# Optimization experiments

Measured on AMD Instinct MI355X. Metric: run time of the kernel, lower is better.

The kernel has to match this reference:

```python
import jax, jax.numpy as jnp
import numpy as np

B, C, L = 4, 256, 2048
HEADS, DIM_HEAD = 8, 64
HIDDEN = HEADS * DIM_HEAD  # 512


def setup_inputs() -> dict:
    key = jax.random.key(0)
    k1, k2, k3, k4 = jax.random.split(key, 4)
    x = jax.random.normal(k1, (B, C, L), dtype=jnp.float32)
    # Conv1d kernel_size=1 weights, squeezed to [out_ch, in_ch]
    w_qkv = jax.random.normal(k2, (3 * HIDDEN, C), dtype=jnp.float32) * (1.0 / np.sqrt(C))
    w_out = jax.random.normal(k3, (C, HIDDEN), dtype=jnp.float32) * (1.0 / np.sqrt(HIDDEN))
    b_out = jax.random.normal(k4, (C,), dtype=jnp.float32) * 0.01
    return {"x": x, "w_qkv": w_qkv, "w_out": w_out, "b_out": b_out}


def reference(x, w_qkv, w_out, b_out):
    b, c, l = x.shape
    scale = DIM_HEAD ** (-0.5)
    # pointwise conv == channel matmul
    qkv = jnp.einsum('oc,bcl->bol', w_qkv, x)  # [b, 3*hidden, l]
    q, k, v = jnp.split(qkv, 3, axis=1)        # each [b, hidden, l]
    def to_heads(t):
        return t.reshape(b, HEADS, DIM_HEAD, l)  # b h d l
    q, k, v = to_heads(q), to_heads(k), to_heads(v)
    q = q * scale
    sim = jnp.einsum('bhdi,bhdj->bhij', q, k)   # [b,h,l,l]
    attn = jax.nn.softmax(sim, axis=-1)          # stable softmax (max-subtract inside)
    out = jnp.einsum('bhij,bhdj->bhid', attn, v)  # [b,h,l,d]
    out = out.transpose(0, 1, 3, 2).reshape(b, HIDDEN, l)  # b (h d) l
    return jnp.einsum('oc,bcl->bol', w_out, out) + b_out[None, :, None]
```

## Files before the change

kernel.cpp:

```cpp
#include <hip/hip_runtime.h>

typedef unsigned short u16;
typedef unsigned int u32;
typedef __bf16 bf16x8 __attribute__((ext_vector_type(8)));
typedef float f32x4 __attribute__((ext_vector_type(4)));
typedef float f32x16 __attribute__((ext_vector_type(16)));

#define MFMA16(a, b, c) __builtin_amdgcn_mfma_f32_16x16x32_bf16((a), (b), (c), 0, 0, 0)
#define MFMA32(a, b, c) __builtin_amdgcn_mfma_f32_32x32x16_bf16((a), (b), (c), 0, 0, 0)

#define Bn 4
#define Cn 256
#define Ln 2048
#define Hn 8
#define Dn 64
#define HID 512

__device__ __forceinline__ u16 bf16_rne(float f) {
  u32 u = __builtin_bit_cast(u32, f);
  u += 0x7FFFu + ((u >> 16) & 1u);
  return (u16)(u >> 16);
}

__device__ __forceinline__ unsigned pack2(float a, float b) {
  return (unsigned)bf16_rne(a) | ((unsigned)bf16_rne(b) << 16);
}

__device__ __forceinline__ u32 pk_hi(float lo, float hi) {
  u32 a = __builtin_bit_cast(u32, lo) + 0x8000u;
  u32 b = __builtin_bit_cast(u32, hi) + 0x8000u;
  return (b & 0xFFFF0000u) | (a >> 16);
}

__device__ __forceinline__ float fast_exp2(float x) {
#if __has_builtin(__builtin_amdgcn_exp2f)
  return __builtin_amdgcn_exp2f(x);
#else
  return exp2f(x);
#endif
}

__device__ __forceinline__ float fast_rcp(float x) {
#if __has_builtin(__builtin_amdgcn_rcpf)
  return __builtin_amdgcn_rcpf(x);
#else
  return 1.0f / x;
#endif
}

__global__ __launch_bounds__(256) void prep_all(const float* __restrict__ wqkv,
                                                const float* __restrict__ wout,
                                                const float* __restrict__ x,
                                                u16* __restrict__ wq,
                                                u16* __restrict__ wo,
                                                u16* __restrict__ xT) {
  const int t = threadIdx.x;
  if (blockIdx.x < 2048) {
    int i = blockIdx.x * 256 + t;
    const float QSCALE = 0.125f * 1.44269504088896340736f;
    if (i < 3 * HID * Cn) {
      float v = wqkv[i];
      if (i < HID * Cn) v *= QSCALE;
      wq[i] = bf16_rne(v);
    } else {
      int j = i - 3 * HID * Cn;
      wo[j] = bf16_rne(wout[j]);
    }
    return;
  }
  __shared__ u16 tile[64][72];
  int v = blockIdx.x - 2048;
  const int lt = v & 31, ct = (v >> 5) & 3, b = v >> 7;
  const float* xp = x + ((size_t)b * Cn + ct * 64) * Ln + lt * 64;
  for (int pass = 0; pass < 4; ++pass) {
    int c = pass * 16 + (t >> 4);
    int l4 = (t & 15) * 4;
    float4 vf = *(const float4*)(xp + (size_t)c * Ln + l4);
    tile[l4 + 0][c] = bf16_rne(vf.x);
    tile[l4 + 1][c] = bf16_rne(vf.y);
    tile[l4 + 2][c] = bf16_rne(vf.z);
    tile[l4 + 3][c] = bf16_rne(vf.w);
  }
  __syncthreads();
  u16* op = xT + ((size_t)b * Ln + lt * 64) * Cn + ct * 64;
  for (int pass = 0; pass < 2; ++pass) {
    int id = pass * 256 + t;
    int l = id >> 3, c8 = (id & 7) * 8;
    *(uint4*)(op + (size_t)l * Cn + c8) = *(const uint4*)&tile[l][c8];
  }
}

__global__ __launch_bounds__(256) void qkv_gemm(const u16* __restrict__ wq,
                                                const u16* __restrict__ xT,
                                                u16* __restrict__ qT,
                                                u16* __restrict__ kT,
                                                u16* __restrict__ vv) {
  __shared__ u16 As[4096];
  __shared__ u16 Bs[4096];
  const int t = threadIdx.x;
  const int nt = blockIdx.x, mt = blockIdx.y, b = blockIdx.z;
  const int m0 = mt * 64, n0 = nt * 64;
  const int w = t >> 6, lane = t & 63, q = lane >> 4, ln = lane & 15;

  const u16* Ag = wq + (size_t)m0 * Cn;
  const u16* Bg = xT + ((size_t)b * Ln + n0) * Cn;

  f32x4 zf = {0.f, 0.f, 0.f, 0.f};
  f32x4 acc[4];
  for (int i = 0; i < 4; ++i) acc[i] = zf;

  const int pr0 = w * 8 + (lane >> 3), pr1 = (4 + w) * 8 + (lane >> 3);
  const int pc0 = (lane & 7) ^ (pr0 & 7), pc1 = (lane & 7) ^ (pr1 & 7);
  const u16* Aad0 = Ag + (size_t)pr0 * Cn + pc0 * 8;
  const u16* Aad1 = Ag + (size_t)pr1 * Cn + pc1 * 8;
  const u16* Bad0 = Bg + (size_t)pr0 * Cn + pc0 * 8;
  const u16* Bad1 = Bg + (size_t)pr1 * Cn + pc1 * 8;

#define LOADAB(kk, A0, A1, B0, B1)               \
  {                                              \
    int k0_ = (kk) * 64;                         \
    A0 = *(const uint4*)(Aad0 + k0_);            \
    A1 = *(const uint4*)(Aad1 + k0_);            \
    B0 = *(const uint4*)(Bad0 + k0_);            \
    B1 = *(const uint4*)(Bad1 + k0_);            \
  }
#define STOREAB(A0, A1, B0, B1)                  \
  {                                              \
    *(uint4*)&As[w * 512 + lane * 8] = A0;       \
    *(uint4*)&As[(4 + w) * 512 + lane * 8] = A1; \
    *(uint4*)&Bs[w * 512 + lane * 8] = B0;       \
    *(uint4*)&Bs[(4 + w) * 512 + lane * 8] = B1; \
  }
#define COMPUTEC()                                                             \
  {                                                                            \
    int ar = w * 16 + ln;                                                      \
    bf16x8 a0 = *(const bf16x8*)&As[ar * 64 + ((q ^ (ln & 7)) * 8)];           \
    bf16x8 a1 = *(const bf16x8*)&As[ar * 64 + (((q + 4) ^ (ln & 7)) * 8)];     \
    for (int n2 = 0; n2 < 4; ++n2) {                                           \
      int br = n2 * 16 + ln;                                                   \
      bf16x8 b0 = *(const bf16x8*)&Bs[br * 64 + ((q ^ (ln & 7)) * 8)];         \
      bf16x8 b1 = *(const bf16x8*)&Bs[br * 64 + (((q + 4) ^ (ln & 7)) * 8)];   \
      acc[n2] = MFMA16(a0, b0, acc[n2]);                                       \
      acc[n2] = MFMA16(a1, b1, acc[n2]);                                       \
    }                                                                          \
  }

  uint4 aa0, aa1, ba0, ba1, ab0, ab1, bb0, bb1;
  LOADAB(0, aa0, aa1, ba0, ba1);
  for (int kk = 0; kk < 4; kk += 2) {
    if (kk) __syncthreads();
    STOREAB(aa0, aa1, ba0, ba1);
    __syncthreads();
    LOADAB(kk + 1, ab0, ab1, bb0, bb1);
    COMPUTEC();
    __syncthreads();
    STOREAB(ab0, ab1, bb0, bb1);
    __syncthreads();
    if (kk + 2 < 4) LOADAB(kk + 2, aa0, aa1, ba0, ba1);
    COMPUTEC();
  }
#undef LOADAB
#undef STOREAB
#undef COMPUTEC

  __syncthreads();
  if (mt < 16) {
    int od0 = w * 16 + q * 4;
    int cw = od0 >> 3, lo = od0 & 7;
    for (int n2 = 0; n2 < 4; ++n2) {
      int l = n2 * 16 + ln;
      uint2 pk;
      pk.x = pack2(acc[n2][0], acc[n2][1]);
      pk.y = pack2(acc[n2][2], acc[n2][3]);
      *(uint2*)&As[l * 64 + ((cw ^ (l & 7)) * 8) + lo] = pk;
    }
    __syncthreads();
    u16* dst = (mt < 8) ? qT + (((size_t)b * Hn + mt) * Ln + n0) * Dn
                        : kT + (((size_t)b * Hn + (mt - 8)) * Ln + n0) * Dn;
    for (int pass = 0; pass < 2; ++pass) {
      int id = pass * 256 + t;
      int l = id >> 3, c = id & 7;
      *(uint4*)(dst + (size_t)l * Dn + c * 8) =
          *(const uint4*)&As[l * 64 + ((c ^ (l & 7)) * 8)];
    }
  } else {
    for (int n2 = 0; n2 < 4; ++n2) {
      int l = n2 * 16 + ln;
      int cl = l >> 3, lo = l & 7;
      for (int r = 0; r < 4; ++r) {
        int od = w * 16 + q * 4 + r;
        As[od * 64 + ((cl ^ (od & 7)) * 8) + lo] = bf16_rne(acc[n2][r]);
      }
    }
    __syncthreads();
    u16* dst = vv + ((size_t)b * HID + (mt - 16) * 64) * Ln + n0;
    for (int pass = 0; pass < 2; ++pass) {
      int id = pass * 256 + t;
      int od = id >> 3, c = id & 7;
      *(uint4*)(dst + (size_t)od * Ln + c * 8) =
          *(const uint4*)&As[od * 64 + ((c ^ (od & 7)) * 8)];
    }
  }
}

__global__ __launch_bounds__(256) void attention(const u16* __restrict__ qT,
                                                 const u16* __restrict__ kT,
                                                 const u16* __restrict__ vv,
                                                 u16* __restrict__ attT) {
  __shared__ u16 Kt[4096];
  __shared__ u16 Vt[4096];
  __shared__ u16 Ps[8192];
  const int t = threadIdx.x;
  const int qb = blockIdx.x, bh = blockIdx.y;
  const int b = bh >> 3, hh = bh & 7;
  const int w = t >> 6, lane = t & 63;
  const int li = lane & 31, h = lane >> 5;
  const int i0 = qb * 128 + w * 32;

  bf16x8 qf0, qf1, qf2, qf3;
  {
    const u16* qrow = qT + (((size_t)bh) * Ln + i0 + li) * Dn + h * 8;
    qf0 = *(const bf16x8*)(qrow + 0);
    qf1 = *(const bf16x8*)(qrow + 16);
    qf2 = *(const bf16x8*)(qrow + 32);
    qf3 = *(const bf16x8*)(qrow + 48);
  }

  const u16* ksrc0 = kT + ((size_t)bh) * Ln * Dn;
  const u16* vsrc0 = vv + ((size_t)b * HID + hh * Dn) * Ln;

  f32x16 o0, o1;
#pragma unroll
  for (int r = 0; r < 16; ++r) { o0[r] = 0.f; o1[r] = 0.f; }
  float lp = 0.f;
  u16* pw = Ps + w * 2048;

  const int pr0 = w * 8 + (lane >> 3), pr1 = (4 + w) * 8 + (lane >> 3);
  const int pc0 = (lane & 7) ^ (pr0 & 7), pc1 = (lane & 7) ^ (pr1 & 7);
  const u16* kadr0 = ksrc0 + (size_t)pr0 * Dn + pc0 * 8;
  const u16* kadr1 = ksrc0 + (size_t)pr1 * Dn + pc1 * 8;
  const u16* vadr0 = vsrc0 + (size_t)pr0 * Ln + pc0 * 8;
  const u16* vadr1 = vsrc0 + (size_t)pr1 * Ln + pc1 * 8;

#define LOADKV(jt, K0, K1, V0, V1)                              \
  {                                                             \
    int j0_ = (jt) * 64;                                        \
    K0 = *(const uint4*)(kadr0 + (size_t)j0_ * Dn);             \
    K1 = *(const uint4*)(kadr1 + (size_t)j0_ * Dn);             \
    V0 = *(const uint4*)(vadr0 + j0_);                          \
    V1 = *(const uint4*)(vadr1 + j0_);                          \
  }
#define STOREKV(K0, K1, V0, V1)                                 \
  {                                                             \
    *(uint4*)&Kt[w * 512 + lane * 8] = K0;                      \
    *(uint4*)&Kt[(4 + w) * 512 + lane * 8] = K1;                \
    *(uint4*)&Vt[w * 512 + lane * 8] = V0;                      \
    *(uint4*)&Vt[(4 + w) * 512 + lane * 8] = V1;                \
  }

#define COMPUTE()                                                              \
  {                                                                            \
    f32x16 sv0, sv1;                                                           \
    _Pragma("unroll") for (int r = 0; r < 16; ++r) { sv0[r] = 0.f; sv1[r] = 0.f; } \
    _Pragma("unroll") for (int c = 0; c < 4; ++c) {                            \
      int ch = 2 * c + h;                                                      \
      bf16x8 k0 = *(const bf16x8*)&Kt[li * 64 + ((ch ^ (li & 7)) * 8)];        \
      bf16x8 k1 = *(const bf16x8*)&Kt[(32 + li) * 64 + ((ch ^ (li & 7)) * 8)]; \
      bf16x8 qc = (c == 0) ? qf0 : (c == 1) ? qf1 : (c == 2) ? qf2 : qf3;      \
      sv0 = MFMA32(k0, qc, sv0);                                               \
      sv1 = MFMA32(k1, qc, sv1);                                               \
    }                                                                          \
    _Pragma("unroll") for (int js = 0; js < 2; ++js) {                         \
      _Pragma("unroll") for (int g = 0; g < 4; ++g) {                          \
        float e0 = fast_exp2(js ? sv1[4 * g + 0] : sv0[4 * g + 0]);            \
        float e1 = fast_exp2(js ? sv1[4 * g + 1] : sv0[4 * g + 1]);            \
        float e2 = fast_exp2(js ? sv1[4 * g + 2] : sv0[4 * g + 2]);            \
        float e3 = fast_exp2(js ? sv1[4 * g + 3] : sv0[4 * g + 3]);            \
        lp += (e0 + e1) + (e2 + e3);                                           \
        uint2 pk;                                                              \
        pk.x = pk_hi(e0, e1);                                                  \
        pk.y = pk_hi(e2, e3);                                                  \
        int cjj = js * 4 + g;                                                  \
        *(uint2*)&pw[li * 64 + ((cjj ^ (li & 7)) * 8) + 4 * h] = pk;           \
      }                                                                        \
    }                                                                          \
    bf16x8 pf0 = *(const bf16x8*)&pw[li * 64 + (((2 * 0 + h) ^ (li & 7)) * 8)];\
    bf16x8 pf1 = *(const bf16x8*)&pw[li * 64 + (((2 * 1 + h) ^ (li & 7)) * 8)];\
    bf16x8 pf2 = *(const bf16x8*)&pw[li * 64 + (((2 * 2 + h) ^ (li & 7)) * 8)];\
    bf16x8 pf3 = *(const bf16x8*)&pw[li * 64 + (((2 * 3 + h) ^ (li & 7)) * 8)];\
    _Pragma("unroll") for (int jc = 0; jc < 4; ++jc) {                         \
      int ch = 2 * jc + h;                                                     \
      bf16x8 pf = (jc == 0) ? pf0 : (jc == 1) ? pf1 : (jc == 2) ? pf2 : pf3;   \
      bf16x8 vf0 = *(const bf16x8*)&Vt[li * 64 + ((ch ^ (li & 7)) * 8)];       \
      bf16x8 vf1 = *(const bf16x8*)&Vt[(32 + li) * 64 + ((ch ^ (li & 7)) * 8)];\
      o0 = MFMA32(pf, vf0, o0);                                                \
      o1 = MFMA32(pf, vf1, o1);                                                \
    }                                                                          \
  }

  uint4 ka0, ka1, wa0, wa1, kb0, kb1, wb0, wb1;
  LOADKV(0, ka0, ka1, wa0, wa1);
  for (int jt = 0; jt < 32; jt += 2) {
    if (jt) __syncthreads();
    STOREKV(ka0, ka1, wa0, wa1);
    __syncthreads();
    LOADKV(jt + 1, kb0, kb1, wb0, wb1);
    COMPUTE();
    __syncthreads();
    STOREKV(kb0, kb1, wb0, wb1);
    __syncthreads();
    if (jt + 2 < 32) LOADKV(jt + 2, ka0, ka1, wa0, wa1);
    COMPUTE();
  }
#undef LOADKV
#undef STOREKV
#undef COMPUTE

  float lsum = lp + __shfl_xor(lp, 32);
  float linv = fast_rcp(lsum);
#pragma unroll
  for (int r = 0; r < 16; ++r) {
    int ir = (r & 3) + 8 * (r >> 2) + 4 * h;
    float lv = __shfl(linv, ir);
    size_t base = ((size_t)b * Ln + i0 + ir) * HID + hh * Dn + li;
    attT[base] = bf16_rne(o0[r] * lv);
    attT[base + 32] = bf16_rne(o1[r] * lv);
  }
}

__global__ __launch_bounds__(256) void out_gemm(const u16* __restrict__ wo,
                                                const u16* __restrict__ attT,
                                                const float* __restrict__ bout,
                                                float* __restrict__ out) {
  __shared__ u16 As[4096];
  __shared__ u16 Bs[4096];
  const int t = threadIdx.x;
  const int nt = blockIdx.x, mt = blockIdx.y, b = blockIdx.z;
  const int m0 = mt * 64, n0 = nt * 64;
  const int w = t >> 6, lane = t & 63, q = lane >> 4, ln = lane & 15;

  const u16* Ag = wo + (size_t)m0 * HID;
  const u16* Bg = attT + ((size_t)b * Ln + n0) * HID;

  f32x4 zf = {0.f, 0.f, 0.f, 0.f};
  f32x4 acc[4];
  for (int i = 0; i < 4; ++i) acc[i] = zf;

  const int pr0 = w * 8 + (lane >> 3), pr1 = (4 + w) * 8 + (lane >> 3);
  const int pc0 = (lane & 7) ^ (pr0 & 7), pc1 = (lane & 7) ^ (pr1 & 7);
  const u16* Aad0 = Ag + (size_t)pr0 * HID + pc0 * 8;
  const u16* Aad1 = Ag + (size_t)pr1 * HID + pc1 * 8;
  const u16* Bad0 = Bg + (size_t)pr0 * HID + pc0 * 8;
  const u16* Bad1 = Bg + (size_t)pr1 * HID + pc1 * 8;

#define LOADAB(kk, A0, A1, B0, B1)               \
  {                                              \
    int k0_ = (kk) * 64;                         \
    A0 = *(const uint4*)(Aad0 + k0_);            \
    A1 = *(const uint4*)(Aad1 + k0_);            \
    B0 = *(const uint4*)(Bad0 + k0_);            \
    B1 = *(const uint4*)(Bad1 + k0_);            \
  }
#define STOREAB(A0, A1, B0, B1)                  \
  {                                              \
    *(uint4*)&As[w * 512 + lane * 8] = A0;       \
    *(uint4*)&As[(4 + w) * 512 + lane * 8] = A1; \
    *(uint4*)&Bs[w * 512 + lane * 8] = B0;       \
    *(uint4*)&Bs[(4 + w) * 512 + lane * 8] = B1; \
  }
#define COMPUTEC()                                                             \
  {                                                                            \
    int ar = w * 16 + ln;                                                      \
    bf16x8 a0 = *(const bf16x8*)&As[ar * 64 + ((q ^ (ln & 7)) * 8)];           \
    bf16x8 a1 = *(const bf16x8*)&As[ar * 64 + (((q + 4) ^ (ln & 7)) * 8)];     \
    for (int n2 = 0; n2 < 4; ++n2) {                                           \
      int br = n2 * 16 + ln;                                                   \
      bf16x8 b0 = *(const bf16x8*)&Bs[br * 64 + ((q ^ (ln & 7)) * 8)];         \
      bf16x8 b1 = *(const bf16x8*)&Bs[br * 64 + (((q + 4) ^ (ln & 7)) * 8)];   \
      acc[n2] = MFMA16(a0, b0, acc[n2]);                                       \
      acc[n2] = MFMA16(a1, b1, acc[n2]);                                       \
    }                                                                          \
  }

  uint4 aa0, aa1, ba0, ba1, ab0, ab1, bb0, bb1;
  LOADAB(0, aa0, aa1, ba0, ba1);
  for (int kk = 0; kk < 8; kk += 2) {
    if (kk) __syncthreads();
    STOREAB(aa0, aa1, ba0, ba1);
    __syncthreads();
    LOADAB(kk + 1, ab0, ab1, bb0, bb1);
    COMPUTEC();
    __syncthreads();
    STOREAB(ab0, ab1, bb0, bb1);
    __syncthreads();
    if (kk + 2 < 8) LOADAB(kk + 2, aa0, aa1, ba0, ba1);
    COMPUTEC();
  }
#undef LOADAB
#undef STOREAB
#undef COMPUTEC

  float bias[4];
  for (int r = 0; r < 4; ++r) bias[r] = bout[m0 + w * 16 + q * 4 + r];
  for (int n2 = 0; n2 < 4; ++n2) {
    int l = n0 + n2 * 16 + ln;
    for (int r = 0; r < 4; ++r) {
      int o = m0 + w * 16 + q * 4 + r;
      out[((size_t)b * Cn + o) * Ln + l] = acc[n2][r] + bias[r];
    }
  }
}

extern "C" void kernel_launch(void* const* d_in, const int* in_sizes, int n_in,
                              void* d_out, int out_size, void* d_ws, size_t ws_size,
                              hipStream_t stream) {
  const float* x = (const float*)d_in[0];
  const float* wqkv = (const float*)d_in[1];
  const float* wout = (const float*)d_in[2];
  const float* bout = (const float*)d_in[3];
  float* out = (float*)d_out;
  char* ws = (char*)d_ws;

  u16* wq_b = (u16*)(ws + 0);
  u16* wo_b = (u16*)(ws + 786432);
  u16* xT   = (u16*)(ws + 1048576);
  u16* qT   = (u16*)(ws + 5242880);
  u16* kT   = (u16*)(ws + 13631488);
  u16* vv   = (u16*)(ws + 22020096);
  u16* attT = (u16*)(ws + 30408704);

  prep_all<<<2560, 256, 0, stream>>>(wqkv, wout, x, wq_b, wo_b, xT);
  qkv_gemm<<<dim3(32, 24, 4), 256, 0, stream>>>(wq_b, xT, qT, kT, vv);
  attention<<<dim3(16, 32), 256, 0, stream>>>(qT, kT, vv, attT);
  out_gemm<<<dim3(32, 4, 4), 256, 0, stream>>>(wo_b, attT, bout, out);
}
```

Before: 142.6 us.

## Split attention keys across segments, fuse QKV per head, use async LDS loads

Attention is split over two key segments (grid z=2), each writing unnormalized bf16 partial outputs and row sums, and a new combine kernel adds and normalizes them. The intent is to fill more CUs than the 512-block grid did. The QKV GEMM now computes Q, K and V for one head in a single block, sharing the x tile, and loads tiles with global_load_lds async copies. The out GEMM uses narrower N tiles for more blocks, and launch bounds and workspace aliasing are adjusted. The trade-offs are an extra kernel launch, partial outputs rounded to bf16 before they are summed, and single-buffered loads with a barrier after each tile.

```diff
diff --git a/kernel.cpp b/kernel.cpp
--- a/kernel.cpp
+++ b/kernel.cpp
@@ -15,6 +15,7 @@
 #define Hn 8
 #define Dn 64
 #define HID 512
+#define SEGELEMS 4194304
 
 __device__ __forceinline__ u16 bf16_rne(float f) {
   u32 u = __builtin_bit_cast(u32, f);
@@ -26,10 +27,19 @@
   return (unsigned)bf16_rne(a) | ((unsigned)bf16_rne(b) << 16);
 }
 
-__device__ __forceinline__ u32 pk_hi(float lo, float hi) {
+__device__ __forceinline__ u32 pkperm(float lo, float hi) {
   u32 a = __builtin_bit_cast(u32, lo) + 0x8000u;
   u32 b = __builtin_bit_cast(u32, hi) + 0x8000u;
+#if __has_builtin(__builtin_amdgcn_perm)
+  return __builtin_amdgcn_perm(b, a, 0x07060302u);
+#else
   return (b & 0xFFFF0000u) | (a >> 16);
+#endif
+}
+
+__device__ __forceinline__ float bf16_up(u16 v) {
+  u32 u = ((u32)v) << 16;
+  return __builtin_bit_cast(float, u);
 }
 
 __device__ __forceinline__ float fast_exp2(float x) {
@@ -46,6 +56,12 @@
 #else
   return 1.0f / x;
 #endif
+}
+
+__device__ __forceinline__ void async_load16(const u16* g, u16* l) {
+  __builtin_amdgcn_global_load_lds(
+      (const __attribute__((address_space(1))) void*)g,
+      (__attribute__((address_space(3))) void*)l, 16, 0, 0);
 }
 
 __global__ __launch_bounds__(256) void prep_all(const float* __restrict__ wqkv,
@@ -90,128 +106,132 @@
   }
 }
 
-__global__ __launch_bounds__(256) void qkv_gemm(const u16* __restrict__ wq,
-                                                const u16* __restrict__ xT,
-                                                u16* __restrict__ qT,
-                                                u16* __restrict__ kT,
-                                                u16* __restrict__ vv) {
-  __shared__ u16 As[4096];
+__global__ __launch_bounds__(256, 4) void qkv_gemm(const u16* __restrict__ wq,
+                                                   const u16* __restrict__ xT,
+                                                   u16* __restrict__ qT,
+                                                   u16* __restrict__ kT,
+                                                   u16* __restrict__ vv) {
   __shared__ u16 Bs[4096];
+  __shared__ u16 Aq[4096];
+  __shared__ u16 Ak[4096];
+  __shared__ u16 Av[4096];
   const int t = threadIdx.x;
-  const int nt = blockIdx.x, mt = blockIdx.y, b = blockIdx.z;
-  const int m0 = mt * 64, n0 = nt * 64;
+  const int nt = blockIdx.x, head = blockIdx.y, b = blockIdx.z;
+  const int n0 = nt * 64, m0 = head * 64;
   const int w = t >> 6, lane = t & 63, q = lane >> 4, ln = lane & 15;
 
-  const u16* Ag = wq + (size_t)m0 * Cn;
   const u16* Bg = xT + ((size_t)b * Ln + n0) * Cn;
+  const u16* AgQ = wq + (size_t)m0 * Cn;
+  const u16* AgK = wq + (size_t)(512 + m0) * Cn;
+  const u16* AgV = wq + (size_t)(1024 + m0) * Cn;
 
   f32x4 zf = {0.f, 0.f, 0.f, 0.f};
-  f32x4 acc[4];
-  for (int i = 0; i < 4; ++i) acc[i] = zf;
+  f32x4 accQ[4], accK[4], accV[4];
+  for (int i = 0; i < 4; ++i) { accQ[i] = zf; accK[i] = zf; accV[i] = zf; }
 
   const int pr0 = w * 8 + (lane >> 3), pr1 = (4 + w) * 8 + (lane >> 3);
   const int pc0 = (lane & 7) ^ (pr0 & 7), pc1 = (lane & 7) ^ (pr1 & 7);
-  const u16* Aad0 = Ag + (size_t)pr0 * Cn + pc0 * 8;
-  const u16* Aad1 = Ag + (size_t)pr1 * Cn + pc1 * 8;
-  const u16* Bad0 = Bg + (size_t)pr0 * Cn + pc0 * 8;
-  const u16* Bad1 = Bg + (size_t)pr1 * Cn + pc1 * 8;
-
-#define LOADAB(kk, A0, A1, B0, B1)               \
-  {                                              \
-    int k0_ = (kk) * 64;                         \
-    A0 = *(const uint4*)(Aad0 + k0_);            \
-    A1 = *(const uint4*)(Aad1 + k0_);            \
-    B0 = *(const uint4*)(Bad0 + k0_);            \
-    B1 = *(const uint4*)(Bad1 + k0_);            \
-  }
-#define STOREAB(A0, A1, B0, B1)                  \
-  {                                              \
-    *(uint4*)&As[w * 512 + lane * 8] = A0;       \
-    *(uint4*)&As[(4 + w) * 512 + lane * 8] = A1; \
-    *(uint4*)&Bs[w * 512 + lane * 8] = B0;       \
-    *(uint4*)&Bs[(4 + w) * 512 + lane * 8] = B1; \
-  }
-#define COMPUTEC()                                                             \
-  {                                                                            \
-    int ar = w * 16 + ln;                                                      \
-    bf16x8 a0 = *(const bf16x8*)&As[ar * 64 + ((q ^ (ln & 7)) * 8)];           \
-    bf16x8 a1 = *(const bf16x8*)&As[ar * 64 + (((q + 4) ^ (ln & 7)) * 8)];     \
-    for (int n2 = 0; n2 < 4; ++n2) {                                           \
-      int br = n2 * 16 + ln;                                                   \
-      bf16x8 b0 = *(const bf16x8*)&Bs[br * 64 + ((q ^ (ln & 7)) * 8)];         \
-      bf16x8 b1 = *(const bf16x8*)&Bs[br * 64 + (((q + 4) ^ (ln & 7)) * 8)];   \
-      acc[n2] = MFMA16(a0, b0, acc[n2]);                                       \
-      acc[n2] = MFMA16(a1, b1, acc[n2]);                                       \
-    }                                                                          \
-  }
-
-  uint4 aa0, aa1, ba0, ba1, ab0, ab1, bb0, bb1;
-  LOADAB(0, aa0, aa1, ba0, ba1);
-  for (int kk = 0; kk < 4; kk += 2) {
-    if (kk) __syncthreads();
-    STOREAB(aa0, aa1, ba0, ba1);
-    __syncthreads();
-    LOADAB(kk + 1, ab0, ab1, bb0, bb1);
-    COMPUTEC();
-    __syncthreads();
-    STOREAB(ab0, ab1, bb0, bb1);
-    __syncthreads();
-    if (kk + 2 < 4) LOADAB(kk + 2, aa0, aa1, ba0, ba1);
-    COMPUTEC();
-  }
-#undef LOADAB
-#undef STOREAB
-#undef COMPUTEC
-
-  __syncthreads();
-  if (mt < 16) {
-    int od0 = w * 16 + q * 4;
-    int cw = od0 >> 3, lo = od0 & 7;
+
+  for (int kk = 0; kk < 4; ++kk) {
+    int k0 = kk * 64;
+    async_load16(Bg + (size_t)pr0 * Cn + k0 + pc0 * 8, &Bs[w * 512]);
+    async_load16(Bg + (size_t)pr1 * Cn + k0 + pc1 * 8, &Bs[(4 + w) * 512]);
+    async_load16(AgQ + (size_t)pr0 * Cn + k0 + pc0 * 8, &Aq[w * 512]);
+    async_load16(AgQ + (size_t)pr1 * Cn + k0 + pc1 * 8, &Aq[(4 + w) * 512]);
+    async_load16(AgK + (size_t)pr0 * Cn + k0 + pc0 * 8, &Ak[w * 512]);
+    async_load16(AgK + (size_t)pr1 * Cn + k0 + pc1 * 8, &Ak[(4 + w) * 512]);
+    async_load16(AgV + (size_t)pr0 * Cn + k0 + pc0 * 8, &Av[w * 512]);
+    async_load16(AgV + (size_t)pr1 * Cn + k0 + pc1 * 8, &Av[(4 + w) * 512]);
+    __syncthreads();
+    int ar = w * 16 + ln;
+    bf16x8 aq0 = *(const bf16x8*)&Aq[ar * 64 + ((q ^ (ln & 7)) * 8)];
+    bf16x8 aq1 = *(const bf16x8*)&Aq[ar * 64 + (((q + 4) ^ (ln & 7)) * 8)];
+    bf16x8 ak0 = *(const bf16x8*)&Ak[ar * 64 + ((q ^ (ln & 7)) * 8)];
+    bf16x8 ak1 = *(const bf16x8*)&Ak[ar * 64 + (((q + 4) ^ (ln & 7)) * 8)];
+    bf16x8 av0 = *(const bf16x8*)&Av[ar * 64 + ((q ^ (ln & 7)) * 8)];
+    bf16x8 av1 = *(const bf16x8*)&Av[ar * 64 + (((q + 4) ^ (ln & 7)) * 8)];
     for (int n2 = 0; n2 < 4; ++n2) {
-      int l = n2 * 16 + ln;
-      uint2 pk;
-      pk.x = pack2(acc[n2][0], acc[n2][1]);
-      pk.y = pack2(acc[n2][2], acc[n2][3]);
-      *(uint2*)&As[l * 64 + ((cw ^ (l & 7)) * 8) + lo] = pk;
-    }
-    __syncthreads();
-    u16* dst = (mt < 8) ? qT + (((size_t)b * Hn + mt) * Ln + n0) * Dn
-                        : kT + (((size_t)b * Hn + (mt - 8)) * Ln + n0) * Dn;
+      int br = n2 * 16 + ln;
+      bf16x8 b0 = *(const bf16x8*)&Bs[br * 64 + ((q ^ (ln & 7)) * 8)];
+      bf16x8 b1 = *(const bf16x8*)&Bs[br * 64 + (((q + 4) ^ (ln & 7)) * 8)];
+      accQ[n2] = MFMA16(aq0, b0, accQ[n2]);
+      accQ[n2] = MFMA16(aq1, b1, accQ[n2]);
+      accK[n2] = MFMA16(ak0, b0, accK[n2]);
+      accK[n2] = MFMA16(ak1, b1, accK[n2]);
+      accV[n2] = MFMA16(av0, b0, accV[n2]);
+      accV[n2] = MFMA16(av1, b1, accV[n2]);
+    }
+    __syncthreads();
+  }
+
+  int od0 = w * 16 + q * 4;
+  int cw = od0 >> 3, lo = od0 & 7;
+  for (int n2 = 0; n2 < 4; ++n2) {
+    int l = n2 * 16 + ln;
+    uint2 pk;
+    pk.x = pack2(accQ[n2][0], accQ[n2][1]);
+    pk.y = pack2(accQ[n2][2], accQ[n2][3]);
+    *(uint2*)&Bs[l * 64 + ((cw ^ (l & 7)) * 8) + lo] = pk;
+  }
+  __syncthreads();
+  {
+    u16* dst = qT + (((size_t)b * Hn + head) * Ln + n0) * Dn;
     for (int pass = 0; pass < 2; ++pass) {
       int id = pass * 256 + t;
       int l = id >> 3, c = id & 7;
       *(uint4*)(dst + (size_t)l * Dn + c * 8) =
-          *(const uint4*)&As[l * 64 + ((c ^ (l & 7)) * 8)];
-    }
-  } else {
-    for (int n2 = 0; n2 < 4; ++n2) {
-      int l = n2 * 16 + ln;
-      int cl = l >> 3, lo = l & 7;
-      for (int r = 0; r < 4; ++r) {
-        int od = w * 16 + q * 4 + r;
-        As[od * 64 + ((cl ^ (od & 7)) * 8) + lo] = bf16_rne(acc[n2][r]);
-      }
-    }
-    __syncthreads();
-    u16* dst = vv + ((size_t)b * HID + (mt - 16) * 64) * Ln + n0;
+          *(const uint4*)&Bs[l * 64 + ((c ^ (l & 7)) * 8)];
+    }
+  }
+  __syncthreads();
+  for (int n2 = 0; n2 < 4; ++n2) {
+    int l = n2 * 16 + ln;
+    uint2 pk;
+    pk.x = pack2(accK[n2][0], accK[n2][1]);
+    pk.y = pack2(accK[n2][2], accK[n2][3]);
+    *(uint2*)&Bs[l * 64 + ((cw ^ (l & 7)) * 8) + lo] = pk;
+  }
+  __syncthreads();
+  {
+    u16* dst = kT + (((size_t)b * Hn + head) * Ln + n0) * Dn;
+    for (int pass = 0; pass < 2; ++pass) {
+      int id = pass * 256 + t;
+      int l = id >> 3, c = id & 7;
+      *(uint4*)(dst + (size_t)l * Dn + c * 8) =
+          *(const uint4*)&Bs[l * 64 + ((c ^ (l & 7)) * 8)];
+    }
+  }
+  __syncthreads();
+  for (int n2 = 0; n2 < 4; ++n2) {
+    int l = n2 * 16 + ln;
+    int cl = l >> 3, lov = l & 7;
+    for (int r = 0; r < 4; ++r) {
+      int od = w * 16 + q * 4 + r;
+      Bs[od * 64 + ((cl ^ (od & 7)) * 8) + lov] = bf16_rne(accV[n2][r]);
+    }
+  }
+  __syncthreads();
+  {
+    u16* dst = vv + ((size_t)b * HID + head * 64) * Ln + n0;
     for (int pass = 0; pass < 2; ++pass) {
       int id = pass * 256 + t;
       int od = id >> 3, c = id & 7;
       *(uint4*)(dst + (size_t)od * Ln + c * 8) =
-          *(const uint4*)&As[od * 64 + ((c ^ (od & 7)) * 8)];
-    }
-  }
-}
-
-__global__ __launch_bounds__(256) void attention(const u16* __restrict__ qT,
-                                                 const u16* __restrict__ kT,
-                                                 const u16* __restrict__ vv,
-                                                 u16* __restrict__ attT) {
+          *(const uint4*)&Bs[od * 64 + ((c ^ (od & 7)) * 8)];
+    }
+  }
+}
+
+__global__ __launch_bounds__(256, 4) void attention(const u16* __restrict__ qT,
+                                                    const u16* __restrict__ kT,
+                                                    const u16* __restrict__ vv,
+                                                    u16* __restrict__ pO,
+                                                    float* __restrict__ lP) {
   __shared__ u16 Kt[4096];
   __shared__ u16 Vt[4096];
   __shared__ u16 Ps[8192];
   const int t = threadIdx.x;
-  const int qb = blockIdx.x, bh = blockIdx.y;
+  const int qb = blockIdx.x, bh = blockIdx.y, seg = blockIdx.z;
   const int b = bh >> 3, hh = bh & 7;
   const int w = t >> 6, lane = t & 63;
   const int li = lane & 31, h = lane >> 5;
@@ -229,151 +249,170 @@
   const u16* ksrc0 = kT + ((size_t)bh) * Ln * Dn;
   const u16* vsrc0 = vv + ((size_t)b * HID + hh * Dn) * Ln;
 
-  f32x16 o0, o1;
-#pragma unroll
-  for (int r = 0; r < 16; ++r) { o0[r] = 0.f; o1[r] = 0.f; }
+  f32x16 z16;
+#pragma unroll
+  for (int r = 0; r < 16; ++r) z16[r] = 0.f;
+  f32x16 o0 = z16, o1 = z16;
   float lp = 0.f;
   u16* pw = Ps + w * 2048;
 
   const int pr0 = w * 8 + (lane >> 3), pr1 = (4 + w) * 8 + (lane >> 3);
   const int pc0 = (lane & 7) ^ (pr0 & 7), pc1 = (lane & 7) ^ (pr1 & 7);
-  const u16* kadr0 = ksrc0 + (size_t)pr0 * Dn + pc0 * 8;
-  const u16* kadr1 = ksrc0 + (size_t)pr1 * Dn + pc1 * 8;
-  const u16* vadr0 = vsrc0 + (size_t)pr0 * Ln + pc0 * 8;
-  const u16* vadr1 = vsrc0 + (size_t)pr1 * Ln + pc1 * 8;
-
-#define LOADKV(jt, K0, K1, V0, V1)                              \
-  {                                                             \
-    int j0_ = (jt) * 64;                                        \
-    K0 = *(const uint4*)(kadr0 + (size_t)j0_ * Dn);             \
-    K1 = *(const uint4*)(kadr1 + (size_t)j0_ * Dn);             \
-    V0 = *(const uint4*)(vadr0 + j0_);                          \
-    V1 = *(const uint4*)(vadr1 + j0_);                          \
-  }
-#define STOREKV(K0, K1, V0, V1)                                 \
-  {                                                             \
-    *(uint4*)&Kt[w * 512 + lane * 8] = K0;                      \
-    *(uint4*)&Kt[(4 + w) * 512 + lane * 8] = K1;                \
-    *(uint4*)&Vt[w * 512 + lane * 8] = V0;                      \
-    *(uint4*)&Vt[(4 + w) * 512 + lane * 8] = V1;                \
-  }
-
-#define COMPUTE()                                                              \
-  {                                                                            \
-    f32x16 sv0, sv1;                                                           \
-    _Pragma("unroll") for (int r = 0; r < 16; ++r) { sv0[r] = 0.f; sv1[r] = 0.f; } \
-    _Pragma("unroll") for (int c = 0; c < 4; ++c) {                            \
-      int ch = 2 * c + h;                                                      \
-      bf16x8 k0 = *(const bf16x8*)&Kt[li * 64 + ((ch ^ (li & 7)) * 8)];        \
-      bf16x8 k1 = *(const bf16x8*)&Kt[(32 + li) * 64 + ((ch ^ (li & 7)) * 8)]; \
-      bf16x8 qc = (c == 0) ? qf0 : (c == 1) ? qf1 : (c == 2) ? qf2 : qf3;      \
-      sv0 = MFMA32(k0, qc, sv0);                                               \
-      sv1 = MFMA32(k1, qc, sv1);                                               \
-    }                                                                          \
-    _Pragma("unroll") for (int js = 0; js < 2; ++js) {                         \
-      _Pragma("unroll") for (int g = 0; g < 4; ++g) {                          \
-        float e0 = fast_exp2(js ? sv1[4 * g + 0] : sv0[4 * g + 0]);            \
-        float e1 = fast_exp2(js ? sv1[4 * g + 1] : sv0[4 * g + 1]);            \
-        float e2 = fast_exp2(js ? sv1[4 * g + 2] : sv0[4 * g + 2]);            \
-        float e3 = fast_exp2(js ? sv1[4 * g + 3] : sv0[4 * g + 3]);            \
-        lp += (e0 + e1) + (e2 + e3);                                           \
-        uint2 pk;                                                              \
-        pk.x = pk_hi(e0, e1);                                                  \
-        pk.y = pk_hi(e2, e3);                                                  \
-        int cjj = js * 4 + g;                                                  \
-        *(uint2*)&pw[li * 64 + ((cjj ^ (li & 7)) * 8) + 4 * h] = pk;           \
-      }                                                                        \
-    }                                                                          \
-    bf16x8 pf0 = *(const bf16x8*)&pw[li * 64 + (((2 * 0 + h) ^ (li & 7)) * 8)];\
-    bf16x8 pf1 = *(const bf16x8*)&pw[li * 64 + (((2 * 1 + h) ^ (li & 7)) * 8)];\
-    bf16x8 pf2 = *(const bf16x8*)&pw[li * 64 + (((2 * 2 + h) ^ (li & 7)) * 8)];\
-    bf16x8 pf3 = *(const bf16x8*)&pw[li * 64 + (((2 * 3 + h) ^ (li & 7)) * 8)];\
-    _Pragma("unroll") for (int jc = 0; jc < 4; ++jc) {                         \
-      int ch = 2 * jc + h;                                                     \
-      bf16x8 pf = (jc == 0) ? pf0 : (jc == 1) ? pf1 : (jc == 2) ? pf2 : pf3;   \
-      bf16x8 vf0 = *(const bf16x8*)&Vt[li * 64 + ((ch ^ (li & 7)) * 8)];       \
-      bf16x8 vf1 = *(const bf16x8*)&Vt[(32 + li) * 64 + ((ch ^ (li & 7)) * 8)];\
-      o0 = MFMA32(pf, vf0, o0);                                                \
-      o1 = MFMA32(pf, vf1, o1);                                                \
-    }                                                                          \
-  }
-
-  uint4 ka0, ka1, wa0, wa1, kb0, kb1, wb0, wb1;
-  LOADKV(0, ka0, ka1, wa0, wa1);
-  for (int jt = 0; jt < 32; jt += 2) {
-    if (jt) __syncthreads();
-    STOREKV(ka0, ka1, wa0, wa1);
-    __syncthreads();
-    LOADKV(jt + 1, kb0, kb1, wb0, wb1);
-    COMPUTE();
-    __syncthreads();
-    STOREKV(kb0, kb1, wb0, wb1);
-    __syncthreads();
-    if (jt + 2 < 32) LOADKV(jt + 2, ka0, ka1, wa0, wa1);
-    COMPUTE();
-  }
-#undef LOADKV
-#undef STOREKV
-#undef COMPUTE
+  const u16* kadr0 = ksrc0 + ((size_t)seg * 1024 + pr0) * Dn + pc0 * 8;
+  const u16* kadr1 = ksrc0 + ((size_t)seg * 1024 + pr1) * Dn + pc1 * 8;
+  const u16* vadr0 = vsrc0 + (size_t)pr0 * Ln + seg * 1024 + pc0 * 8;
+  const u16* vadr1 = vsrc0 + (size_t)pr1 * Ln + seg * 1024 + pc1 * 8;
+
+  const int sw = (li & 7);
+
+  for (int jt = 0; jt < 16; ++jt) {
+    int j0 = jt * 64;
+    async_load16(kadr0 + (size_t)j0 * Dn, &Kt[w * 512]);
+    async_load16(kadr1 + (size_t)j0 * Dn, &Kt[(4 + w) * 512]);
+    async_load16(vadr0 + j0, &Vt[w * 512]);
+    async_load16(vadr1 + j0, &Vt[(4 + w) * 512]);
+    __syncthreads();
+
+    f32x16 sv0, sv1;
+    {
+      bf16x8 k0 = *(const bf16x8*)&Kt[li * 64 + (((0 + h) ^ sw) * 8)];
+      bf16x8 k1 = *(const bf16x8*)&Kt[(32 + li) * 64 + (((0 + h) ^ sw) * 8)];
+      sv0 = MFMA32(k0, qf0, z16);
+      sv1 = MFMA32(k1, qf0, z16);
+    }
+    {
+      bf16x8 k0 = *(const bf16x8*)&Kt[li * 64 + (((2 + h) ^ sw) * 8)];
+      bf16x8 k1 = *(const bf16x8*)&Kt[(32 + li) * 64 + (((2 + h) ^ sw) * 8)];
+      sv0 = MFMA32(k0, qf1, sv0);
+      sv1 = MFMA32(k1, qf1, sv1);
+    }
+    {
+      bf16x8 k0 = *(const bf16x8*)&Kt[li * 64 + (((4 + h) ^ sw) * 8)];
+      bf16x8 k1 = *(const bf16x8*)&Kt[(32 + li) * 64 + (((4 + h) ^ sw) * 8)];
+      sv0 = MFMA32(k0, qf2, sv0);
+      sv1 = MFMA32(k1, qf2, sv1);
+    }
+    {
+      bf16x8 k0 = *(const bf16x8*)&Kt[li * 64 + (((6 + h) ^ sw) * 8)];
+      bf16x8 k1 = *(const bf16x8*)&Kt[(32 + li) * 64 + (((6 + h) ^ sw) * 8)];
+      sv0 = MFMA32(k0, qf3, sv0);
+      sv1 = MFMA32(k1, qf3, sv1);
+    }
+
+#pragma unroll
+    for (int js = 0; js < 2; ++js) {
+#pragma unroll
+      for (int g = 0; g < 4; ++g) {
+        float e0 = fast_exp2(js ? sv1[4 * g + 0] : sv0[4 * g + 0]);
+        float e1 = fast_exp2(js ? sv1[4 * g + 1] : sv0[4 * g + 1]);
+        float e2 = fast_exp2(js ? sv1[4 * g + 2] : sv0[4 * g + 2]);
+        float e3 = fast_exp2(js ? sv1[4 * g + 3] : sv0[4 * g + 3]);
+        lp += (e0 + e1) + (e2 + e3);
+        uint2 pk;
+        pk.x = pkperm(e0, e1);
+        pk.y = pkperm(e2, e3);
+        int cjj = js * 4 + g;
+        *(uint2*)&pw[li * 64 + ((cjj ^ sw) * 8) + 4 * h] = pk;
+      }
+    }
+
+    bf16x8 pf0 = *(const bf16x8*)&pw[li * 64 + (((0 + h) ^ sw) * 8)];
+    bf16x8 pf1 = *(const bf16x8*)&pw[li * 64 + (((2 + h) ^ sw) * 8)];
+    bf16x8 pf2 = *(const bf16x8*)&pw[li * 64 + (((4 + h) ^ sw) * 8)];
+    bf16x8 pf3 = *(const bf16x8*)&pw[li * 64 + (((6 + h) ^ sw) * 8)];
+#pragma unroll
+    for (int jc = 0; jc < 4; ++jc) {
+      int ch = 2 * jc + h;
+      bf16x8 pf = (jc == 0) ? pf0 : (jc == 1) ? pf1 : (jc == 2) ? pf2 : pf3;
+      bf16x8 vf0 = *(const bf16x8*)&Vt[li * 64 + ((ch ^ sw) * 8)];
+      bf16x8 vf1 = *(const bf16x8*)&Vt[(32 + li) * 64 + ((ch ^ sw) * 8)];
+      o0 = MFMA32(pf, vf0, o0);
+      o1 = MFMA32(pf, vf1, o1);
+    }
+    __syncthreads();
+  }
 
   float lsum = lp + __shfl_xor(lp, 32);
-  float linv = fast_rcp(lsum);
+  if (h == 0)
+    lP[(((size_t)seg * Bn + b) * Hn + hh) * Ln + i0 + li] = lsum;
+  u16* po = pO + (size_t)seg * SEGELEMS;
 #pragma unroll
   for (int r = 0; r < 16; ++r) {
     int ir = (r & 3) + 8 * (r >> 2) + 4 * h;
-    float lv = __shfl(linv, ir);
     size_t base = ((size_t)b * Ln + i0 + ir) * HID + hh * Dn + li;
-    attT[base] = bf16_rne(o0[r] * lv);
-    attT[base + 32] = bf16_rne(o1[r] * lv);
-  }
-}
-
-__global__ __launch_bounds__(256) void out_gemm(const u16* __restrict__ wo,
-                                                const u16* __restrict__ attT,
-                                                const float* __restrict__ bout,
-                                                float* __restrict__ out) {
+    po[base] = bf16_rne(o0[r]);
+    po[base + 32] = bf16_rne(o1[r]);
+  }
+}
+
+__global__ __launch_bounds__(256) void combine(const u16* __restrict__ pO,
+                                               const float* __restrict__ lP,
+                                               u16* __restrict__ attT) {
+  int idx8 = (blockIdx.x * 256 + threadIdx.x) * 8;
+  int i_lin = idx8 >> 9;
+  int h = (idx8 & 511) >> 6;
+  int b = i_lin >> 11, i = i_lin & 2047;
+  float l = lP[(b * 8 + h) * 2048 + i] + lP[(32 + b * 8 + h) * 2048 + i];
+  float s = fast_rcp(l);
+  uint4 u0 = *(const uint4*)(pO + idx8);
+  uint4 u1 = *(const uint4*)(pO + SEGELEMS + idx8);
+  u32 a[4] = {u0.x, u0.y, u0.z, u0.w};
+  u32 c[4] = {u1.x, u1.y, u1.z, u1.w};
+  uint4 r;
+  u32 rw[4];
+#pragma unroll
+  for (int k = 0; k < 4; ++k) {
+    float flo = (bf16_up((u16)(a[k] & 0xFFFF)) + bf16_up((u16)(c[k] & 0xFFFF))) * s;
+    float fhi = (bf16_up((u16)(a[k] >> 16)) + bf16_up((u16)(c[k] >> 16))) * s;
+    rw[k] = pack2(flo, fhi);
+  }
+  r.x = rw[0]; r.y = rw[1]; r.z = rw[2]; r.w = rw[3];
+  *(uint4*)(attT + idx8) = r;
+}
+
+__global__ __launch_bounds__(256, 4) void out_gemm(const u16* __restrict__ wo,
+                                                   const u16* __restrict__ attT,
+                                                   const float* __restrict__ bout,
+                                                   float* __restrict__ out) {
   __shared__ u16 As[4096];
-  __shared__ u16 Bs[4096];
+  __shared__ u16 Bs[2048];
   const int t = threadIdx.x;
   const int nt = blockIdx.x, mt = blockIdx.y, b = blockIdx.z;
-  const int m0 = mt * 64, n0 = nt * 64;
+  const int m0 = mt * 64, n0 = nt * 32;
   const int w = t >> 6, lane = t & 63, q = lane >> 4, ln = lane & 15;
 
   const u16* Ag = wo + (size_t)m0 * HID;
   const u16* Bg = attT + ((size_t)b * Ln + n0) * HID;
 
   f32x4 zf = {0.f, 0.f, 0.f, 0.f};
-  f32x4 acc[4];
-  for (int i = 0; i < 4; ++i) acc[i] = zf;
+  f32x4 acc[2];
+  acc[0] = zf; acc[1] = zf;
 
   const int pr0 = w * 8 + (lane >> 3), pr1 = (4 + w) * 8 + (lane >> 3);
   const int pc0 = (lane & 7) ^ (pr0 & 7), pc1 = (lane & 7) ^ (pr1 & 7);
   const u16* Aad0 = Ag + (size_t)pr0 * HID + pc0 * 8;
   const u16* Aad1 = Ag + (size_t)pr1 * HID + pc1 * 8;
   const u16* Bad0 = Bg + (size_t)pr0 * HID + pc0 * 8;
-  const u16* Bad1 = Bg + (size_t)pr1 * HID + pc1 * 8;
-
-#define LOADAB(kk, A0, A1, B0, B1)               \
+
+#define LOADAB(kk, A0, A1, B0)                   \
   {                                              \
     int k0_ = (kk) * 64;                         \
     A0 = *(const uint4*)(Aad0 + k0_);            \
     A1 = *(const uint4*)(Aad1 + k0_);            \
     B0 = *(const uint4*)(Bad0 + k0_);            \
-    B1 = *(const uint4*)(Bad1 + k0_);            \
-  }
-#define STOREAB(A0, A1, B0, B1)                  \
+  }
+#define STOREAB(A0, A1, B0)                      \
   {                                              \
     *(uint4*)&As[w * 512 + lane * 8] = A0;       \
     *(uint4*)&As[(4 + w) * 512 + lane * 8] = A1; \
     *(uint4*)&Bs[w * 512 + lane * 8] = B0;       \
-    *(uint4*)&Bs[(4 + w) * 512 + lane * 8] = B1; \
   }
 #define COMPUTEC()                                                             \
   {                                                                            \
     int ar = w * 16 + ln;                                                      \
     bf16x8 a0 = *(const bf16x8*)&As[ar * 64 + ((q ^ (ln & 7)) * 8)];           \
     bf16x8 a1 = *(const bf16x8*)&As[ar * 64 + (((q + 4) ^ (ln & 7)) * 8)];     \
-    for (int n2 = 0; n2 < 4; ++n2) {                                           \
+    for (int n2 = 0; n2 < 2; ++n2) {                                           \
       int br = n2 * 16 + ln;                                                   \
       bf16x8 b0 = *(const bf16x8*)&Bs[br * 64 + ((q ^ (ln & 7)) * 8)];         \
       bf16x8 b1 = *(const bf16x8*)&Bs[br * 64 + (((q + 4) ^ (ln & 7)) * 8)];   \
@@ -382,18 +421,18 @@
     }                                                                          \
   }
 
-  uint4 aa0, aa1, ba0, ba1, ab0, ab1, bb0, bb1;
-  LOADAB(0, aa0, aa1, ba0, ba1);
+  uint4 aa0, aa1, ba0, ab0, ab1, bb0;
+  LOADAB(0, aa0, aa1, ba0);
   for (int kk = 0; kk < 8; kk += 2) {
     if (kk) __syncthreads();
-    STOREAB(aa0, aa1, ba0, ba1);
-    __syncthreads();
-    LOADAB(kk + 1, ab0, ab1, bb0, bb1);
+    STOREAB(aa0, aa1, ba0);
+    __syncthreads();
+    LOADAB(kk + 1, ab0, ab1, bb0);
     COMPUTEC();
     __syncthreads();
-    STOREAB(ab0, ab1, bb0, bb1);
-    __syncthreads();
-    if (kk + 2 < 8) LOADAB(kk + 2, aa0, aa1, ba0, ba1);
+    STOREAB(ab0, ab1, bb0);
+    __syncthreads();
+    if (kk + 2 < 8) LOADAB(kk + 2, aa0, aa1, ba0);
     COMPUTEC();
   }
 #undef LOADAB
@@ -402,7 +441,7 @@
 
   float bias[4];
   for (int r = 0; r < 4; ++r) bias[r] = bout[m0 + w * 16 + q * 4 + r];
-  for (int n2 = 0; n2 < 4; ++n2) {
+  for (int n2 = 0; n2 < 2; ++n2) {
     int l = n0 + n2 * 16 + ln;
     for (int r = 0; r < 4; ++r) {
       int o = m0 + w * 16 + q * 4 + r;
@@ -421,16 +460,19 @@
   float* out = (float*)d_out;
   char* ws = (char*)d_ws;
 
-  u16* wq_b = (u16*)(ws + 0);
-  u16* wo_b = (u16*)(ws + 786432);
-  u16* xT   = (u16*)(ws + 1048576);
-  u16* qT   = (u16*)(ws + 5242880);
-  u16* kT   = (u16*)(ws + 13631488);
-  u16* vv   = (u16*)(ws + 22020096);
-  u16* attT = (u16*)(ws + 30408704);
+  u16* wq_b  = (u16*)(ws + 0);
+  u16* wo_b  = (u16*)(ws + 786432);
+  float* lP  = (float*)(ws + 1048576);
+  u16* qT    = (u16*)(ws + 1572864);
+  u16* kT    = (u16*)(ws + 9961472);
+  u16* vv    = (u16*)(ws + 18350080);
+  u16* xT    = (u16*)(ws + 26738688);
+  u16* pO    = (u16*)(ws + 26738688);
+  u16* attT  = qT;
 
   prep_all<<<2560, 256, 0, stream>>>(wqkv, wout, x, wq_b, wo_b, xT);
-  qkv_gemm<<<dim3(32, 24, 4), 256, 0, stream>>>(wq_b, xT, qT, kT, vv);
-  attention<<<dim3(16, 32), 256, 0, stream>>>(qT, kT, vv, attT);
-  out_gemm<<<dim3(32, 4, 4), 256, 0, stream>>>(wo_b, attT, bout, out);
-}
+  qkv_gemm<<<dim3(32, 8, 4), 256, 0, stream>>>(wq_b, xT, qT, kT, vv);
+  attention<<<dim3(16, 32, 2), 256, 0, stream>>>(qT, kT, vv, pO, lP);
+  combine<<<2048, 256, 0, stream>>>(pO, lP, attT);
+  out_gemm<<<dim3(64, 4, 4), 256, 0, stream>>>(wo_b, attT, bout, out);
+}
```

Measured after the change: 140.7 us. No clear change (-1.3%).
